# Kernel tuning notes

Hardware: AMD Instinct MI355X
Metric: run time of the kernel (lower is better)

The kernel has to match this reference:

```python
import jax, jax.numpy as jnp
import numpy as np

B, M, L, D = 4, 4, 512, 1024
N_HEAD = 16
D_HEAD = D // N_HEAD
LN_EPS = 1e-6


def setup_inputs() -> dict:
    key = jax.random.key(0)
    ks = jax.random.split(key, 9)
    s = 1.0 / np.sqrt(D)
    return {
        "q": jax.random.normal(ks[0], (B, M, L, D), dtype=jnp.float32),
        "k": jax.random.normal(ks[1], (B, M, L, D), dtype=jnp.float32),
        "qi": jax.random.normal(ks[2], (B, M, L, D), dtype=jnp.float32),
        "mask": jax.random.randint(ks[3], (B, M, L, L), 0, 2, dtype=jnp.int32),
        "w_qs": jax.random.normal(ks[4], (D, D), dtype=jnp.float32) * s,
        "w_qis": jax.random.normal(ks[5], (D, D), dtype=jnp.float32) * s,
        "w_fc": jax.random.normal(ks[6], (D, D), dtype=jnp.float32) * s,
        "ln_g": jnp.ones((D,), dtype=jnp.float32),
        "ln_b": jnp.zeros((D,), dtype=jnp.float32),
    }


def _l2_normalize(x):
    # normaliseE: divide by sqrt(sum of squares) over the last axis (no eps)
    return x / jnp.sqrt(jnp.sum(x * x, axis=-1, keepdims=True))


def _softmax2d(attn):
    # softmax jointly over the (doc, key) axes = axes (1, 4) of [B,M,H,Lq,Lk]
    m = jnp.max(attn, axis=(1, 4), keepdims=True)
    e = jnp.exp(attn - m)
    return e / jnp.sum(e, axis=(1, 4), keepdims=True)


def reference(q, k, qi, mask, w_qs, w_qis, w_fc, ln_g, ln_b):
    del k  # unused by the original forward
    b, m, lq, d = q.shape
    residual = q

    # LayerNorm(d_model, eps=1e-6) on q only
    mu = jnp.mean(q, axis=-1, keepdims=True)
    var = jnp.mean(jnp.square(q - mu), axis=-1, keepdims=True)
    qn = (q - mu) / jnp.sqrt(var + LN_EPS) * ln_g + ln_b

    # projections (bias-free) and head split -> [B,M,H,L,d_head]
    qh = (qn @ w_qs).reshape(b, m, lq, N_HEAD, D_HEAD)
    qih = (qi @ w_qis).reshape(b, m, qi.shape[2], N_HEAD, D_HEAD)
    qh = jnp.swapaxes(_l2_normalize(qh), 2, 3)
    qih = jnp.swapaxes(_l2_normalize(qih), 2, 3)

    # cosine-similarity scores (BSM=True -> no temperature scaling)
    attn = jnp.einsum("bmhqd,bmhkd->bmhqk", qh, qih)

    # mask broadcast over heads (the torch transpose dance is equivalent)
    attn = jnp.where(mask[:, :, None, :, :] == 0, -1e9, attn)

    attn = _softmax2d(attn)  # dropout is identity at eval

    out = jnp.einsum("bmhqk,bmhkd->bmhqd", attn, qih)
    out = jnp.swapaxes(out, 2, 3).reshape(b, m, lq, d)
    out = out @ w_fc + residual
    return out, attn
```

## Files before the change

kernel.cpp:

```cpp
#include <hip/hip_runtime.h>
#include <hip/hip_bf16.h>
#include <cstdint>
#include <cstddef>

#define Bq 4
#define Mq 4
#define Lseq 512
#define Dmod 1024
#define Hq 16
#define DHq 64

using bf16 = __bf16;
using bf16x4 = __attribute__((ext_vector_type(4))) __bf16;
using bf16x8 = __attribute__((ext_vector_type(8))) __bf16;
using f32x4 = __attribute__((ext_vector_type(4))) float;
using u64 = unsigned long long;

__device__ __forceinline__ void gld_lds16(const bf16* g, bf16* l) {
  __builtin_amdgcn_global_load_lds(
      (const __attribute__((address_space(1))) void*)g,
      (__attribute__((address_space(3))) void*)l, 16, 0, 0);
}

template <int WAVES_M, int WAVES_N, int WTM, int WTN>
__device__ __forceinline__ void gemm_core(const bf16* __restrict__ A,
                                          const bf16* __restrict__ Bt,
                                          int K, int lda, int ldb,
                                          bf16* As, bf16* Bs,
                                          f32x4 (&acc)[WTM][WTN]) {
  constexpr int BM = WAVES_M * WTM * 16;
  constexpr int BN = WAVES_N * WTN * 16;
  constexpr int IA = BM / 64;
  constexpr int IB = BN / 64;
  constexpr int ASZ = BM * 32;
  constexpr int BSZ = BN * 32;

  const int t = threadIdx.x;
  const int lane = t & 63;
  const int wave = t >> 6;
  const int wm = wave % WAVES_M;
  const int wn = wave / WAVES_M;
  const int r = t >> 2;
  const int c8 = (t & 3) * 8;
  const int fr = lane & 15;
  const int fk = (lane >> 4) * 8;

  const bf16* Ab = A + (size_t)r * lda + c8;
  const bf16* Bb = Bt + (size_t)r * ldb + c8;

#pragma unroll
  for (int i = 0; i < IA; ++i)
    gld_lds16(Ab + (size_t)i * 64 * lda, As + i * 2048 + t * 8);
#pragma unroll
  for (int i = 0; i < IB; ++i)
    gld_lds16(Bb + (size_t)i * 64 * ldb, Bs + i * 2048 + t * 8);

  int cur = 0;
  for (int k0 = 0; k0 < K; k0 += 32) {
    asm volatile("s_waitcnt vmcnt(0)" ::: "memory");
    __syncthreads();

    if (k0 + 32 < K) {
      const int nxt = cur ^ 1;
#pragma unroll
      for (int i = 0; i < IA; ++i)
        gld_lds16(Ab + (size_t)i * 64 * lda + k0 + 32,
                  As + nxt * ASZ + i * 2048 + t * 8);
#pragma unroll
      for (int i = 0; i < IB; ++i)
        gld_lds16(Bb + (size_t)i * 64 * ldb + k0 + 32,
                  Bs + nxt * BSZ + i * 2048 + t * 8);
    }

    const bf16* Ac = As + cur * ASZ;
    const bf16* Bc = Bs + cur * BSZ;
    bf16x8 af[WTM], bfv[WTN];
#pragma unroll
    for (int i = 0; i < WTM; ++i)
      af[i] = *(const bf16x8*)(Ac + (wm * WTM * 16 + i * 16 + fr) * 32 + fk);
#pragma unroll
    for (int j = 0; j < WTN; ++j)
      bfv[j] = *(const bf16x8*)(Bc + (wn * WTN * 16 + j * 16 + fr) * 32 + fk);
    __builtin_amdgcn_s_setprio(1);
#pragma unroll
    for (int i = 0; i < WTM; ++i)
#pragma unroll
      for (int j = 0; j < WTN; ++j)
        acc[i][j] = __builtin_amdgcn_mfma_f32_16x16x32_bf16(af[i], bfv[j],
                                                            acc[i][j], 0, 0, 0);
    __builtin_amdgcn_s_setprio(0);
    cur ^= 1;
  }
}

__global__ __launch_bounds__(256) void gemm_bt_128_l2n(
    const bf16* __restrict__ A, const bf16* __restrict__ Bt,
    bf16* __restrict__ C, int K, int lda, int ldb, int ldc) {
  __shared__ __align__(16) bf16 As[2 * 128 * 32];
  __shared__ __align__(16) bf16 Bs[2 * 128 * 32];
  f32x4 acc[4][4] = {};
  const bf16* Ab = A + (size_t)blockIdx.y * 128 * lda;
  const bf16* Bb = Bt + (size_t)blockIdx.x * 128 * ldb;
  gemm_core<2, 2, 4, 4>(Ab, Bb, K, lda, ldb, As, Bs, acc);

  const int t = threadIdx.x, lane = t & 63, wave = t >> 6;
  const int wm = wave & 1, wn = wave >> 1;
  const int cr = (lane >> 4) * 4, cc = lane & 15;
  const size_t row0 = (size_t)blockIdx.y * 128 + wm * 64;
  const size_t col0 = (size_t)blockIdx.x * 128 + wn * 64;
#pragma unroll
  for (int i = 0; i < 4; ++i)
#pragma unroll
    for (int rg = 0; rg < 4; ++rg) {
      float ss = 0.0f;
#pragma unroll
      for (int j = 0; j < 4; ++j) ss += acc[i][j][rg] * acc[i][j][rg];
      ss += __shfl_xor(ss, 1);
      ss += __shfl_xor(ss, 2);
      ss += __shfl_xor(ss, 4);
      ss += __shfl_xor(ss, 8);
      const float r = (ss > 0.0f) ? rsqrtf(ss) : 0.0f;
#pragma unroll
      for (int j = 0; j < 4; ++j)
        C[(row0 + i * 16 + cr + rg) * ldc + col0 + j * 16 + cc] =
            (bf16)(acc[i][j][rg] * r);
    }
}

__global__ __launch_bounds__(256) void gemm_bt_resid(
    const bf16* __restrict__ A, const bf16* __restrict__ Bt,
    const float* __restrict__ resid, float* __restrict__ C, int K, int lda,
    int ldb, int ldc) {
  __shared__ __align__(16) bf16 As[2 * 128 * 32];
  __shared__ __align__(16) bf16 Bs[2 * 128 * 32];
  f32x4 acc[4][4] = {};
  const bf16* Ab = A + (size_t)blockIdx.y * 128 * lda;
  const bf16* Bb = Bt + (size_t)blockIdx.x * 128 * ldb;
  gemm_core<2, 2, 4, 4>(Ab, Bb, K, lda, ldb, As, Bs, acc);

  const int t = threadIdx.x, lane = t & 63, wave = t >> 6;
  const int wm = wave & 1, wn = wave >> 1;
  const int cr = (lane >> 4) * 4, cc = lane & 15;
  const size_t row0 = (size_t)blockIdx.y * 128 + wm * 64;
  const size_t col0 = (size_t)blockIdx.x * 128 + wn * 64;
#pragma unroll
  for (int i = 0; i < 4; ++i)
#pragma unroll
    for (int j = 0; j < 4; ++j)
#pragma unroll
      for (int rg = 0; rg < 4; ++rg) {
        size_t idx = (row0 + i * 16 + cr + rg) * ldc + col0 + j * 16 + cc;
        float rv = __builtin_nontemporal_load(resid + idx);
        __builtin_nontemporal_store(acc[i][j][rg] + rv, C + idx);
      }
}

__global__ __launch_bounds__(256) void mask_to_bits(
    const int* __restrict__ mask, u64* __restrict__ mb) {
  const int wid = blockIdx.x * 4 + (threadIdx.x >> 6);
  const int lane = threadIdx.x & 63;
#pragma unroll
  for (int it = 0; it < 16; ++it) {
    const size_t W = (size_t)wid * 16 + it;
    const u64 b = __ballot(mask[W * 64 + lane] != 0);
    if (lane == 0) mb[W] = b;
  }
}

__device__ __forceinline__ void attn_swizzle(int flat, int& z, int& q0) {
  const int slot = flat >> 3;
  z = (flat & 7) * 32 + (slot >> 2);
  q0 = (slot & 3) * 128;
}

__global__ __launch_bounds__(256) void denom_kernel(
    const bf16* __restrict__ qh, const bf16* __restrict__ qih,
    const u64* __restrict__ mb, float* __restrict__ denom) {
  __shared__ __align__(16) bf16 Qs[128 * 64];
  __shared__ __align__(16) bf16 Ks[2][64 * 64];

  int z, q0;
  attn_swizzle(blockIdx.x, z, q0);
  const int bm = z >> 4, h = z & 15;

  const int t = threadIdx.x;
  const int lane = t & 63;
  const int wave = t >> 6;
  const int wm = wave & 1, wn = wave >> 1;
  const int fr = lane & 15;
  const int hi = lane >> 4;
  const int sr = t >> 3;
  const int sc = t & 7;

  const bf16* qh_b = qh + ((size_t)bm * Lseq + q0) * Dmod + h * DHq;
  const bf16* qih_b = qih + (size_t)bm * Lseq * Dmod + h * DHq;
  const u64* mrow = mb + (size_t)bm * Lseq * 8;

#pragma unroll
  for (int s = 0; s < 4; ++s) {
    const int r = s * 32 + sr;
    gld_lds16(qh_b + (size_t)r * Dmod + ((sc ^ (r & 7)) << 3),
              Qs + s * 2048 + t * 8);
  }
#pragma unroll
  for (int s = 0; s < 2; ++s) {
    const int r = s * 32 + sr;
    gld_lds16(qih_b + (size_t)r * Dmod + ((sc ^ (r & 7)) << 3),
              Ks[0] + s * 2048 + t * 8);
  }

  float racc[4][4] = {};

  for (int kt = 0; kt < 8; ++kt) {
    asm volatile("s_waitcnt vmcnt(0)" ::: "memory");
    __syncthreads();

    if (kt < 7) {
      const int kv1 = (kt + 1) * 64;
#pragma unroll
      for (int s = 0; s < 2; ++s) {
        const int r = s * 32 + sr;
        gld_lds16(qih_b + (size_t)(kv1 + r) * Dmod + ((sc ^ (r & 7)) << 3),
                  Ks[(kt + 1) & 1] + s * 2048 + t * 8);
      }
    }

    u64 mw[4][4];
#pragma unroll
    for (int i = 0; i < 4; ++i)
#pragma unroll
      for (int rg = 0; rg < 4; ++rg)
        mw[i][rg] =
            mrow[(size_t)(q0 + wm * 64 + i * 16 + hi * 4 + rg) * 8 + kt];

    const bf16* Kc = Ks[kt & 1];
    f32x4 acc_s[4][2] = {};
    __builtin_amdgcn_s_setprio(1);
#pragma unroll
    for (int kk = 0; kk < 2; ++kk) {
      bf16x8 bq[4], bk[2];
#pragma unroll
      for (int i = 0; i < 4; ++i) {
        const int row = wm * 64 + i * 16 + fr;
        bq[i] = *(const bf16x8*)(Qs + row * 64 +
                                 ((((kk << 2) + hi) ^ (row & 7)) << 3));
      }
#pragma unroll
      for (int j = 0; j < 2; ++j) {
        const int row = wn * 32 + j * 16 + fr;
        bk[j] = *(const bf16x8*)(Kc + row * 64 +
                                 ((((kk << 2) + hi) ^ (row & 7)) << 3));
      }
#pragma unroll
      for (int i = 0; i < 4; ++i)
#pragma unroll
        for (int j = 0; j < 2; ++j)
          acc_s[i][j] = __builtin_amdgcn_mfma_f32_16x16x32_bf16(
              bq[i], bk[j], acc_s[i][j], 0, 0, 0);
    }
    __builtin_amdgcn_s_setprio(0);

#pragma unroll
    for (int i = 0; i < 4; ++i)
#pragma unroll
      for (int rg = 0; rg < 4; ++rg) {
        const unsigned hw = (unsigned)(mw[i][rg] >> (wn * 32));
#pragma unroll
        for (int j = 0; j < 2; ++j)
          if ((hw >> (j * 16 + fr)) & 1)
            racc[i][rg] += __expf(acc_s[i][j][rg] - 1.0f);
      }
  }

  float* dp = denom + ((size_t)(bm >> 2) * Hq + h) * Lseq + q0 + wm * 64;
#pragma unroll
  for (int i = 0; i < 4; ++i)
#pragma unroll
    for (int rg = 0; rg < 4; ++rg) {
      float rs = racc[i][rg];
      rs += __shfl_xor(rs, 1);
      rs += __shfl_xor(rs, 2);
      rs += __shfl_xor(rs, 4);
      rs += __shfl_xor(rs, 8);
      if (fr == 0) atomicAdd(dp + i * 16 + hi * 4 + rg, rs);
    }
}

__global__ __launch_bounds__(256) void fused_attn(
    const bf16* __restrict__ qh, const bf16* __restrict__ qih,
    const bf16* __restrict__ qih_t, const u64* __restrict__ mb,
    const float* __restrict__ denom, float* __restrict__ attn,
    bf16* __restrict__ outh) {
  __shared__ __align__(16) bf16 Qs[128 * 64];
  __shared__ __align__(16) bf16 Ks[2][64 * 64];
  __shared__ __align__(16) bf16 Vs[2][64 * 64];
  __shared__ __align__(16) bf16 Ps[2][128 * 64];

  int z, q0;
  attn_swizzle(blockIdx.x, z, q0);
  const int bm = z >> 4, h = z & 15;

  const int t = threadIdx.x;
  const int lane = t & 63;
  const int wave = t >> 6;
  const int wm = wave & 1, wn = wave >> 1;
  const int fr = lane & 15;
  const int hi = lane >> 4;
  const int sr = t >> 3;
  const int sc = t & 7;

  const bf16* qh_b = qh + ((size_t)bm * Lseq + q0) * Dmod + h * DHq;
  const bf16* qih_b = qih + (size_t)bm * Lseq * Dmod + h * DHq;
  const bf16* vt_b = qih_t + (size_t)z * DHq * Lseq;
  const u64* mrow = mb + (size_t)bm * Lseq * 8;
  float* arow = attn + (size_t)z * Lseq * Lseq;

#pragma unroll
  for (int s = 0; s < 4; ++s) {
    const int r = s * 32 + sr;
    gld_lds16(qh_b + (size_t)r * Dmod + ((sc ^ (r & 7)) << 3),
              Qs + s * 2048 + t * 8);
  }
#pragma unroll
  for (int s = 0; s < 2; ++s) {
    const int r = s * 32 + sr;
    gld_lds16(qih_b + (size_t)r * Dmod + ((sc ^ (r & 7)) << 3),
              Ks[0] + s * 2048 + t * 8);
    gld_lds16(vt_b + (size_t)r * Lseq + ((sc ^ (r & 7)) << 3),
              Vs[0] + s * 2048 + t * 8);
  }

  const float* drow = denom + ((size_t)(bm >> 2) * Hq + h) * Lseq + q0;
  float invd[4][4];
#pragma unroll
  for (int i = 0; i < 4; ++i)
#pragma unroll
    for (int rg = 0; rg < 4; ++rg) {
      const float d = drow[wm * 64 + i * 16 + hi * 4 + rg];
      invd[i][rg] = (d > 0.0f) ? 1.0f / d : 0.0f;
    }

  f32x4 acc_o[4][2] = {};

  for (int kt = 0; kt < 8; ++kt) {
    const int kv0 = kt * 64;
    asm volatile("s_waitcnt vmcnt(0)" ::: "memory");
    __syncthreads();

    if (kt < 7) {
      const int kv1 = kv0 + 64;
#pragma unroll
      for (int s = 0; s < 2; ++s) {
        const int r = s * 32 + sr;
        gld_lds16(qih_b + (size_t)(kv1 + r) * Dmod + ((sc ^ (r & 7)) << 3),
                  Ks[(kt + 1) & 1] + s * 2048 + t * 8);
        gld_lds16(vt_b + (size_t)r * Lseq + kv1 + ((sc ^ (r & 7)) << 3),
                  Vs[(kt + 1) & 1] + s * 2048 + t * 8);
      }
    }

    u64 mw[4][4];
#pragma unroll
    for (int i = 0; i < 4; ++i)
#pragma unroll
      for (int rg = 0; rg < 4; ++rg)
        mw[i][rg] =
            mrow[(size_t)(q0 + wm * 64 + i * 16 + hi * 4 + rg) * 8 + kt];

    const bf16* Kc = Ks[kt & 1];
    f32x4 acc_s[4][2] = {};
    __builtin_amdgcn_s_setprio(1);
#pragma unroll
    for (int kk = 0; kk < 2; ++kk) {
      bf16x8 bq[4], bk[2];
#pragma unroll
      for (int i = 0; i < 4; ++i) {
        const int row = wm * 64 + i * 16 + fr;
        bq[i] = *(const bf16x8*)(Qs + row * 64 +
                                 ((((kk << 2) + hi) ^ (row & 7)) << 3));
      }
#pragma unroll
      for (int j = 0; j < 2; ++j) {
        const int row = wn * 32 + j * 16 + fr;
        bk[j] = *(const bf16x8*)(Kc + row * 64 +
                                 ((((kk << 2) + hi) ^ (row & 7)) << 3));
      }
#pragma unroll
      for (int i = 0; i < 4; ++i)
#pragma unroll
        for (int j = 0; j < 2; ++j)
          acc_s[i][j] = __builtin_amdgcn_mfma_f32_16x16x32_bf16(
              bq[i], bk[j], acc_s[i][j], 0, 0, 0);
    }
    __builtin_amdgcn_s_setprio(0);

    bf16* Pc = Ps[kt & 1];
#pragma unroll
    for (int i = 0; i < 4; ++i)
#pragma unroll
      for (int j = 0; j < 2; ++j)
#pragma unroll
        for (int rg = 0; rg < 4; ++rg) {
          const int ql = wm * 64 + i * 16 + hi * 4 + rg;
          const int cl = wn * 32 + j * 16 + fr;
          const unsigned hw = (unsigned)(mw[i][rg] >> (wn * 32));
          float p = 0.0f;
          if ((hw >> (j * 16 + fr)) & 1)
            p = __expf(acc_s[i][j][rg] - 1.0f) * invd[i][rg];
          __builtin_nontemporal_store(
              p, arow + (size_t)(q0 + ql) * Lseq + kv0 + cl);
          Pc[ql * 64 + (((cl >> 3) ^ (ql & 7)) << 3) + (cl & 7)] = (bf16)p;
        }
    asm volatile("s_waitcnt lgkmcnt(0)" ::: "memory");
    __builtin_amdgcn_s_barrier();

    const bf16* Vc = Vs[kt & 1];
    __builtin_amdgcn_s_setprio(1);
#pragma unroll
    for (int kk = 0; kk < 2; ++kk) {
      bf16x8 ap[4], bv[2];
#pragma unroll
      for (int i = 0; i < 4; ++i) {
        const int row = wm * 64 + i * 16 + fr;
        ap[i] = *(const bf16x8*)(Pc + row * 64 +
                                 ((((kk << 2) + hi) ^ (row & 7)) << 3));
      }
#pragma unroll
      for (int j = 0; j < 2; ++j) {
        const int row = wn * 32 + j * 16 + fr;
        bv[j] = *(const bf16x8*)(Vc + row * 64 +
                                 ((((kk << 2) + hi) ^ (row & 7)) << 3));
      }
#pragma unroll
      for (int i = 0; i < 4; ++i)
#pragma unroll
        for (int j = 0; j < 2; ++j)
          acc_o[i][j] = __builtin_amdgcn_mfma_f32_16x16x32_bf16(
              ap[i], bv[j], acc_o[i][j], 0, 0, 0);
    }
    __builtin_amdgcn_s_setprio(0);
  }

  bf16* Cb = outh + ((size_t)bm * Lseq + q0) * Dmod + h * DHq;
#pragma unroll
  for (int i = 0; i < 4; ++i)
#pragma unroll
    for (int j = 0; j < 2; ++j)
#pragma unroll
      for (int rg = 0; rg < 4; ++rg)
        Cb[(size_t)(wm * 64 + i * 16 + hi * 4 + rg) * Dmod + wn * 32 +
           j * 16 + fr] = (bf16)acc_o[i][j][rg];
}

__global__ __launch_bounds__(256) void ln_kernel(const float* __restrict__ q,
                                                 const float* __restrict__ g,
                                                 const float* __restrict__ b,
                                                 bf16* __restrict__ qn) {
  const size_t row = blockIdx.x;
  const float* x = q + row * Dmod;
  bf16* y = qn + row * Dmod;
  const int t = threadIdx.x;
  float4 v = *(const float4*)(x + t * 4);
  float s = v.x + v.y + v.z + v.w;
  float ss = v.x * v.x + v.y * v.y + v.z * v.z + v.w * v.w;
  for (int off = 32; off; off >>= 1) {
    s += __shfl_xor(s, off);
    ss += __shfl_xor(ss, off);
  }
  __shared__ float sm[8];
  const int wave = t >> 6, lane = t & 63;
  if (lane == 0) { sm[wave * 2] = s; sm[wave * 2 + 1] = ss; }
  __syncthreads();
  s = sm[0] + sm[2] + sm[4] + sm[6];
  ss = sm[1] + sm[3] + sm[5] + sm[7];
  const float mean = s * (1.0f / Dmod);
  const float var = ss * (1.0f / Dmod) - mean * mean;
  const float rstd = rsqrtf(var + 1e-6f);
  float4 gg = *(const float4*)(g + t * 4);
  float4 bb = *(const float4*)(b + t * 4);
  bf16x4 o;
  o[0] = (bf16)((v.x - mean) * rstd * gg.x + bb.x);
  o[1] = (bf16)((v.y - mean) * rstd * gg.y + bb.y);
  o[2] = (bf16)((v.z - mean) * rstd * gg.z + bb.z);
  o[3] = (bf16)((v.w - mean) * rstd * gg.w + bb.w);
  *(bf16x4*)(y + t * 4) = o;
}

__global__ __launch_bounds__(256) void cvt_f32_bf16(const float* __restrict__ in,
                                                    bf16* __restrict__ out) {
  const size_t i = ((size_t)blockIdx.x * 256 + threadIdx.x) * 4;
  float4 v = *(const float4*)(in + i);
  bf16x4 o;
  o[0] = (bf16)v.x; o[1] = (bf16)v.y; o[2] = (bf16)v.z; o[3] = (bf16)v.w;
  *(bf16x4*)(out + i) = o;
}

__global__ __launch_bounds__(256) void transpose64_f32(
    const float* __restrict__ in, bf16* __restrict__ out, int ld_in,
    int ld_out) {
  __shared__ bf16 tile[64 * 65];
  const int r0 = blockIdx.y * 64, c0 = blockIdx.x * 64;
  const int t = threadIdx.x, cl = t & 63, rq = t >> 6;
#pragma unroll
  for (int it = 0; it < 16; ++it) {
    const int rl = it * 4 + rq;
    tile[cl * 65 + rl] = (bf16)in[(size_t)(r0 + rl) * ld_in + c0 + cl];
  }
  __syncthreads();
#pragma unroll
  for (int it = 0; it < 16; ++it) {
    const int ol = it * 4 + rq;
    out[(size_t)(c0 + ol) * ld_out + r0 + cl] = tile[ol * 65 + cl];
  }
}

__global__ __launch_bounds__(256) void transpose_qih(
    const bf16* __restrict__ qih, bf16* __restrict__ qih_t) {
  __shared__ bf16 tile[64 * 65];
  const int z = blockIdx.z;
  const int bm = z >> 4, h = z & 15;
  const bf16* in = qih + (size_t)bm * Lseq * Dmod + h * DHq;
  bf16* out = qih_t + (size_t)z * DHq * Lseq;
  const int r0 = blockIdx.x * 64;
  const int t = threadIdx.x, cl = t & 63, rq = t >> 6;
#pragma unroll
  for (int it = 0; it < 16; ++it) {
    const int rl = it * 4 + rq;
    tile[cl * 65 + rl] = in[(size_t)(r0 + rl) * Dmod + cl];
  }
  __syncthreads();
#pragma unroll
  for (int it = 0; it < 16; ++it) {
    const int dh = it * 4 + rq;
    out[(size_t)dh * Lseq + r0 + cl] = tile[dh * 65 + cl];
  }
}

extern "C" void kernel_launch(void* const* d_in, const int* in_sizes, int n_in,
                              void* d_out, int out_size, void* d_ws,
                              size_t ws_size, hipStream_t stream) {
  const float* q = (const float*)d_in[0];
  const float* qi = (const float*)d_in[2];
  const int* mask = (const int*)d_in[3];
  const float* w_qs = (const float*)d_in[4];
  const float* w_qis = (const float*)d_in[5];
  const float* w_fc = (const float*)d_in[6];
  const float* ln_g = (const float*)d_in[7];
  const float* ln_b = (const float*)d_in[8];

  float* out = (float*)d_out;
  const size_t NE = (size_t)Bq * Mq * Lseq * Dmod;
  float* attn = out + NE;

  char* attnc = (char*)attn;
  bf16* qib = (bf16*)attnc;
  bf16* wqs_t = (bf16*)(attnc + (16u << 20));
  bf16* wqis_t = (bf16*)(attnc + (18u << 20));

  char* ws = (char*)d_ws;
  const size_t SZ = NE * sizeof(bf16);
  bf16* qn = (bf16*)(ws);
  bf16* qh = (bf16*)(ws + SZ);
  bf16* qih = (bf16*)(ws + 2 * SZ);
  bf16* qih_t = (bf16*)(ws + 3 * SZ);
  bf16* wfc_t = (bf16*)(ws + 4 * SZ);
  float* denom = (float*)(ws + 4 * SZ + (2u << 20));
  u64* mbits = (u64*)(ws + 4 * SZ + (4u << 20));
  bf16* outh = qn;

  const int ROWS = Bq * Mq * Lseq;

  mask_to_bits<<<1024, 256, 0, stream>>>(mask, mbits);
  cvt_f32_bf16<<<NE / 1024, 256, 0, stream>>>(qi, qib);
  transpose64_f32<<<dim3(16, 16), 256, 0, stream>>>(w_qs, wqs_t, Dmod, Dmod);
  transpose64_f32<<<dim3(16, 16), 256, 0, stream>>>(w_qis, wqis_t, Dmod, Dmod);
  transpose64_f32<<<dim3(16, 16), 256, 0, stream>>>(w_fc, wfc_t, Dmod, Dmod);
  hipMemsetAsync(denom, 0, (size_t)Bq * Hq * Lseq * sizeof(float), stream);

  ln_kernel<<<ROWS, 256, 0, stream>>>(q, ln_g, ln_b, qn);

  gemm_bt_128_l2n<<<dim3(Dmod / 128, ROWS / 128), 256, 0, stream>>>(
      qn, wqs_t, qh, Dmod, Dmod, Dmod, Dmod);
  gemm_bt_128_l2n<<<dim3(Dmod / 128, ROWS / 128), 256, 0, stream>>>(
      qib, wqis_t, qih, Dmod, Dmod, Dmod, Dmod);

  transpose_qih<<<dim3(Lseq / 64, 1, Bq * Mq * Hq), 256, 0, stream>>>(qih,
                                                                      qih_t);

  denom_kernel<<<1024, 256, 0, stream>>>(qh, qih, mbits, denom);

  fused_attn<<<1024, 256, 0, stream>>>(qh, qih, qih_t, mbits, denom, attn,
                                       outh);

  gemm_bt_resid<<<dim3(Dmod / 128, ROWS / 128), 256, 0, stream>>>(
      outh, wfc_t, q, out, Dmod, Dmod, Dmod, Dmod);
}
```

Baseline: 581.9 us.

## Merge prep kernels, batch both projection GEMMs, fuse qih transpose into epilogue

Merges layer norm, mask bit-packing, the three weight transposes and the qi conversion into one prep kernel that dispatches on block index. Runs the two projection GEMMs as a single launch using the z grid dimension. The qi projection epilogue also writes the per-head transposed qih through an LDS tile, which removes the separate transpose kernel and its reread of qih. This cuts several launches and one global pass over qih, at the cost of extra LDS use and barriers in the GEMM epilogue, which may lower occupancy.

```diff
diff --git a/kernel.cpp b/kernel.cpp
--- a/kernel.cpp
+++ b/kernel.cpp
@@ -93,21 +93,32 @@
   }
 }
 
-__global__ __launch_bounds__(256) void gemm_bt_128_l2n(
-    const bf16* __restrict__ A, const bf16* __restrict__ Bt,
-    bf16* __restrict__ C, int K, int lda, int ldb, int ldc) {
+__global__ __launch_bounds__(256) void gemm_proj(
+    const bf16* __restrict__ A0, const bf16* __restrict__ B0,
+    bf16* __restrict__ C0, const bf16* __restrict__ A1,
+    const bf16* __restrict__ B1, bf16* __restrict__ C1,
+    bf16* __restrict__ qih_t) {
   __shared__ __align__(16) bf16 As[2 * 128 * 32];
   __shared__ __align__(16) bf16 Bs[2 * 128 * 32];
+  __shared__ __align__(16) bf16 Ts[64 * 140];
+
+  const int zz = blockIdx.z;
+  const bf16* A = zz ? A1 : A0;
+  const bf16* Bt = zz ? B1 : B0;
+  bf16* C = zz ? C1 : C0;
+
   f32x4 acc[4][4] = {};
-  const bf16* Ab = A + (size_t)blockIdx.y * 128 * lda;
-  const bf16* Bb = Bt + (size_t)blockIdx.x * 128 * ldb;
-  gemm_core<2, 2, 4, 4>(Ab, Bb, K, lda, ldb, As, Bs, acc);
+  gemm_core<2, 2, 4, 4>(A + (size_t)blockIdx.y * 128 * Dmod,
+                        Bt + (size_t)blockIdx.x * 128 * Dmod, Dmod, Dmod,
+                        Dmod, As, Bs, acc);
 
   const int t = threadIdx.x, lane = t & 63, wave = t >> 6;
   const int wm = wave & 1, wn = wave >> 1;
   const int cr = (lane >> 4) * 4, cc = lane & 15;
   const size_t row0 = (size_t)blockIdx.y * 128 + wm * 64;
   const size_t col0 = (size_t)blockIdx.x * 128 + wn * 64;
+
+  float rinv[4][4];
 #pragma unroll
   for (int i = 0; i < 4; ++i)
 #pragma unroll
@@ -119,12 +130,39 @@
       ss += __shfl_xor(ss, 2);
       ss += __shfl_xor(ss, 4);
       ss += __shfl_xor(ss, 8);
-      const float r = (ss > 0.0f) ? rsqrtf(ss) : 0.0f;
+      rinv[i][rg] = (ss > 0.0f) ? rsqrtf(ss) : 0.0f;
 #pragma unroll
       for (int j = 0; j < 4; ++j)
-        C[(row0 + i * 16 + cr + rg) * ldc + col0 + j * 16 + cc] =
-            (bf16)(acc[i][j][rg] * r);
-    }
+        C[(row0 + i * 16 + cr + rg) * Dmod + col0 + j * 16 + cc] =
+            (bf16)(acc[i][j][rg] * rinv[i][rg]);
+    }
+
+  if (zz) {
+    const int bm = (int)(blockIdx.y >> 2);
+    const int lq0 = ((int)blockIdx.y & 3) * 128;
+#pragma unroll
+    for (int hh = 0; hh < 2; ++hh) {
+      __syncthreads();
+      if (wn == hh) {
+#pragma unroll
+        for (int i = 0; i < 4; ++i)
+#pragma unroll
+          for (int j = 0; j < 4; ++j)
+#pragma unroll
+            for (int rg = 0; rg < 4; ++rg)
+              Ts[(j * 16 + cc) * 140 + wm * 64 + i * 16 + cr + rg] =
+                  (bf16)(acc[i][j][rg] * rinv[i][rg]);
+      }
+      __syncthreads();
+      const int h = 2 * (int)blockIdx.x + hh;
+      bf16* op = qih_t + ((size_t)(bm * Hq + h) * DHq) * Lseq;
+      const int dh = t >> 2, c0 = (t & 3) * 32;
+#pragma unroll
+      for (int v = 0; v < 4; ++v)
+        *(bf16x8*)(op + (size_t)dh * Lseq + lq0 + c0 + v * 8) =
+            *(const bf16x8*)(Ts + dh * 140 + c0 + v * 8);
+    }
+  }
 }
 
 __global__ __launch_bounds__(256) void gemm_bt_resid(
@@ -155,15 +193,82 @@
       }
 }
 
-__global__ __launch_bounds__(256) void mask_to_bits(
-    const int* __restrict__ mask, u64* __restrict__ mb) {
-  const int wid = blockIdx.x * 4 + (threadIdx.x >> 6);
-  const int lane = threadIdx.x & 63;
-#pragma unroll
-  for (int it = 0; it < 16; ++it) {
-    const size_t W = (size_t)wid * 16 + it;
-    const u64 b = __ballot(mask[W * 64 + lane] != 0);
-    if (lane == 0) mb[W] = b;
+__global__ __launch_bounds__(256) void prep_kernel(
+    const float* __restrict__ q, const float* __restrict__ g,
+    const float* __restrict__ bb_, bf16* __restrict__ qn,
+    const int* __restrict__ mask, u64* __restrict__ mb,
+    const float* __restrict__ w_qs, bf16* __restrict__ wqs_t,
+    const float* __restrict__ w_qis, bf16* __restrict__ wqis_t,
+    const float* __restrict__ w_fc, bf16* __restrict__ wfc_t,
+    const float* __restrict__ qi, bf16* __restrict__ qib) {
+  __shared__ float sm[8];
+  __shared__ bf16 tile[64 * 65];
+  const int b = blockIdx.x;
+  const int t = threadIdx.x;
+
+  if (b < 8192) {
+    const size_t row = b;
+    const float* x = q + row * Dmod;
+    bf16* y = qn + row * Dmod;
+    float4 v = *(const float4*)(x + t * 4);
+    float s = v.x + v.y + v.z + v.w;
+    float ss = v.x * v.x + v.y * v.y + v.z * v.z + v.w * v.w;
+    for (int off = 32; off; off >>= 1) {
+      s += __shfl_xor(s, off);
+      ss += __shfl_xor(ss, off);
+    }
+    const int wave = t >> 6, lane = t & 63;
+    if (lane == 0) { sm[wave * 2] = s; sm[wave * 2 + 1] = ss; }
+    __syncthreads();
+    s = sm[0] + sm[2] + sm[4] + sm[6];
+    ss = sm[1] + sm[3] + sm[5] + sm[7];
+    const float mean = s * (1.0f / Dmod);
+    const float var = ss * (1.0f / Dmod) - mean * mean;
+    const float rstd = rsqrtf(var + 1e-6f);
+    float4 gg = *(const float4*)(g + t * 4);
+    float4 bv = *(const float4*)(bb_ + t * 4);
+    bf16x4 o;
+    o[0] = (bf16)((v.x - mean) * rstd * gg.x + bv.x);
+    o[1] = (bf16)((v.y - mean) * rstd * gg.y + bv.y);
+    o[2] = (bf16)((v.z - mean) * rstd * gg.z + bv.z);
+    o[3] = (bf16)((v.w - mean) * rstd * gg.w + bv.w);
+    *(bf16x4*)(y + t * 4) = o;
+  } else if (b < 9216) {
+    const int wid = (b - 8192) * 4 + (t >> 6);
+    const int lane = t & 63;
+#pragma unroll
+    for (int it = 0; it < 16; ++it) {
+      const size_t W = (size_t)wid * 16 + it;
+      const u64 bits = __ballot(mask[W * 64 + lane] != 0);
+      if (lane == 0) mb[W] = bits;
+    }
+  } else if (b < 9984) {
+    const int which = (b - 9216) >> 8;
+    const int it = (b - 9216) & 255;
+    const float* in = which == 0 ? w_qs : (which == 1 ? w_qis : w_fc);
+    bf16* outp = which == 0 ? wqs_t : (which == 1 ? wqis_t : wfc_t);
+    const int r0 = (it >> 4) * 64, c0 = (it & 15) * 64;
+    const int cl = t & 63, rq = t >> 6;
+#pragma unroll
+    for (int k = 0; k < 16; ++k) {
+      const int rl = k * 4 + rq;
+      tile[cl * 65 + rl] = (bf16)in[(size_t)(r0 + rl) * Dmod + c0 + cl];
+    }
+    __syncthreads();
+#pragma unroll
+    for (int k = 0; k < 16; ++k) {
+      const int ol = k * 4 + rq;
+      outp[(size_t)(c0 + ol) * Dmod + r0 + cl] = tile[ol * 65 + cl];
+    }
+  } else {
+    for (int vb = b - 9984; vb < 8192; vb += 2048) {
+      const size_t i = ((size_t)vb * 256 + t) * 4;
+      float4 v = *(const float4*)(qi + i);
+      bf16x4 o;
+      o[0] = (bf16)v.x; o[1] = (bf16)v.y;
+      o[2] = (bf16)v.z; o[3] = (bf16)v.w;
+      *(bf16x4*)(qib + i) = o;
+    }
   }
 }
 
@@ -452,90 +557,6 @@
            j * 16 + fr] = (bf16)acc_o[i][j][rg];
 }
 
-__global__ __launch_bounds__(256) void ln_kernel(const float* __restrict__ q,
-                                                 const float* __restrict__ g,
-                                                 const float* __restrict__ b,
-                                                 bf16* __restrict__ qn) {
-  const size_t row = blockIdx.x;
-  const float* x = q + row * Dmod;
-  bf16* y = qn + row * Dmod;
-  const int t = threadIdx.x;
-  float4 v = *(const float4*)(x + t * 4);
-  float s = v.x + v.y + v.z + v.w;
-  float ss = v.x * v.x + v.y * v.y + v.z * v.z + v.w * v.w;
-  for (int off = 32; off; off >>= 1) {
-    s += __shfl_xor(s, off);
-    ss += __shfl_xor(ss, off);
-  }
-  __shared__ float sm[8];
-  const int wave = t >> 6, lane = t & 63;
-  if (lane == 0) { sm[wave * 2] = s; sm[wave * 2 + 1] = ss; }
-  __syncthreads();
-  s = sm[0] + sm[2] + sm[4] + sm[6];
-  ss = sm[1] + sm[3] + sm[5] + sm[7];
-  const float mean = s * (1.0f / Dmod);
-  const float var = ss * (1.0f / Dmod) - mean * mean;
-  const float rstd = rsqrtf(var + 1e-6f);
-  float4 gg = *(const float4*)(g + t * 4);
-  float4 bb = *(const float4*)(b + t * 4);
-  bf16x4 o;
-  o[0] = (bf16)((v.x - mean) * rstd * gg.x + bb.x);
-  o[1] = (bf16)((v.y - mean) * rstd * gg.y + bb.y);
-  o[2] = (bf16)((v.z - mean) * rstd * gg.z + bb.z);
-  o[3] = (bf16)((v.w - mean) * rstd * gg.w + bb.w);
-  *(bf16x4*)(y + t * 4) = o;
-}
-
-__global__ __launch_bounds__(256) void cvt_f32_bf16(const float* __restrict__ in,
-                                                    bf16* __restrict__ out) {
-  const size_t i = ((size_t)blockIdx.x * 256 + threadIdx.x) * 4;
-  float4 v = *(const float4*)(in + i);
-  bf16x4 o;
-  o[0] = (bf16)v.x; o[1] = (bf16)v.y; o[2] = (bf16)v.z; o[3] = (bf16)v.w;
-  *(bf16x4*)(out + i) = o;
-}
-
-__global__ __launch_bounds__(256) void transpose64_f32(
-    const float* __restrict__ in, bf16* __restrict__ out, int ld_in,
-    int ld_out) {
-  __shared__ bf16 tile[64 * 65];
-  const int r0 = blockIdx.y * 64, c0 = blockIdx.x * 64;
-  const int t = threadIdx.x, cl = t & 63, rq = t >> 6;
-#pragma unroll
-  for (int it = 0; it < 16; ++it) {
-    const int rl = it * 4 + rq;
-    tile[cl * 65 + rl] = (bf16)in[(size_t)(r0 + rl) * ld_in + c0 + cl];
-  }
-  __syncthreads();
-#pragma unroll
-  for (int it = 0; it < 16; ++it) {
-    const int ol = it * 4 + rq;
-    out[(size_t)(c0 + ol) * ld_out + r0 + cl] = tile[ol * 65 + cl];
-  }
-}
-
-__global__ __launch_bounds__(256) void transpose_qih(
-    const bf16* __restrict__ qih, bf16* __restrict__ qih_t) {
-  __shared__ bf16 tile[64 * 65];
-  const int z = blockIdx.z;
-  const int bm = z >> 4, h = z & 15;
-  const bf16* in = qih + (size_t)bm * Lseq * Dmod + h * DHq;
-  bf16* out = qih_t + (size_t)z * DHq * Lseq;
-  const int r0 = blockIdx.x * 64;
-  const int t = threadIdx.x, cl = t & 63, rq = t >> 6;
-#pragma unroll
-  for (int it = 0; it < 16; ++it) {
-    const int rl = it * 4 + rq;
-    tile[cl * 65 + rl] = in[(size_t)(r0 + rl) * Dmod + cl];
-  }
-  __syncthreads();
-#pragma unroll
-  for (int it = 0; it < 16; ++it) {
-    const int dh = it * 4 + rq;
-    out[(size_t)dh * Lseq + r0 + cl] = tile[dh * 65 + cl];
-  }
-}
-
 extern "C" void kernel_launch(void* const* d_in, const int* in_sizes, int n_in,
                               void* d_out, int out_size, void* d_ws,
                               size_t ws_size, hipStream_t stream) {
@@ -570,22 +591,13 @@
 
   const int ROWS = Bq * Mq * Lseq;
 
-  mask_to_bits<<<1024, 256, 0, stream>>>(mask, mbits);
-  cvt_f32_bf16<<<NE / 1024, 256, 0, stream>>>(qi, qib);
-  transpose64_f32<<<dim3(16, 16), 256, 0, stream>>>(w_qs, wqs_t, Dmod, Dmod);
-  transpose64_f32<<<dim3(16, 16), 256, 0, stream>>>(w_qis, wqis_t, Dmod, Dmod);
-  transpose64_f32<<<dim3(16, 16), 256, 0, stream>>>(w_fc, wfc_t, Dmod, Dmod);
+  prep_kernel<<<12032, 256, 0, stream>>>(q, ln_g, ln_b, qn, mask, mbits,
+                                         w_qs, wqs_t, w_qis, wqis_t, w_fc,
+                                         wfc_t, qi, qib);
   hipMemsetAsync(denom, 0, (size_t)Bq * Hq * Lseq * sizeof(float), stream);
 
-  ln_kernel<<<ROWS, 256, 0, stream>>>(q, ln_g, ln_b, qn);
-
-  gemm_bt_128_l2n<<<dim3(Dmod / 128, ROWS / 128), 256, 0, stream>>>(
-      qn, wqs_t, qh, Dmod, Dmod, Dmod, Dmod);
-  gemm_bt_128_l2n<<<dim3(Dmod / 128, ROWS / 128), 256, 0, stream>>>(
-      qib, wqis_t, qih, Dmod, Dmod, Dmod, Dmod);
-
-  transpose_qih<<<dim3(Lseq / 64, 1, Bq * Mq * Hq), 256, 0, stream>>>(qih,
-                                                                      qih_t);
+  gemm_proj<<<dim3(Dmod / 128, ROWS / 128, 2), 256, 0, stream>>>(
+      qn, wqs_t, qh, qib, wqis_t, qih, qih_t);
 
   denom_kernel<<<1024, 256, 0, stream>>>(qh, qih, mbits, denom);
 
```

After: 564.0 us. 3.1% less time.
